# Optimization experiments

Hardware: AMD Instinct MI355X
Metric: run time of the kernel (lower is better)

The kernel has to match this reference:

```python
import jax, jax.numpy as jnp
import numpy as np

B, C, H, W = 2, 256, 64, 64
HEADS = 8
HEAD_DIM = C // HEADS  # 32
INNER = HEADS * HEAD_DIM  # 256
GROUPS = 32
EPS = 1e-5


def groupnorm(x, w, b):
    # x: [B, C, H, W]; normalize over (C//G, H, W) within each of G groups
    Bx, Cx, Hx, Wx = x.shape
    xg = x.reshape(Bx, GROUPS, -1)
    mu = xg.mean(axis=-1, keepdims=True)
    var = xg.var(axis=-1, keepdims=True)
    xn = ((xg - mu) * jax.lax.rsqrt(var + EPS)).reshape(Bx, Cx, Hx, Wx)
    return xn * w[:, None, None] + b[:, None, None]


def setup_inputs() -> dict:
    key = jax.random.key(0)
    k0, k1, k2 = jax.random.split(key, 3)
    x = jax.random.normal(k0, (B, C, H, W), dtype=jnp.float32)
    gn_weight = jnp.ones((C,), dtype=jnp.float32)
    gn_bias = jnp.zeros((C,), dtype=jnp.float32)
    # 1x1 conv weights (kernel dims squeezed): [out_ch, in_ch]
    w_qkv = jax.random.normal(k1, (3 * INNER, C), dtype=jnp.float32) * 0.02
    w_out = jax.random.normal(k2, (C, INNER), dtype=jnp.float32) * 0.02
    return {"x": x, "gn_weight": gn_weight, "gn_bias": gn_bias,
            "w_qkv": w_qkv, "w_out": w_out}


def reference(x, gn_weight, gn_bias, w_qkv, w_out):
    Bx, Cx, Hx, Wx = x.shape
    N = Hx * Wx
    scale = HEAD_DIM ** -0.5
    xn = groupnorm(x, gn_weight, gn_bias)
    # 1x1 conv == channel matmul
    qkv = jnp.einsum('oc,bchw->bohw', w_qkv, xn)  # [B, 3*INNER, H, W]
    q, k, v = jnp.split(qkv, 3, axis=1)
    # 'b (h d) x y -> b h (x y) d'
    def to_heads(t):
        return t.reshape(Bx, HEADS, HEAD_DIM, N).transpose(0, 1, 3, 2)  # bhnd
    q, k, v = to_heads(q), to_heads(k), to_heads(v)
    sim = jnp.einsum('bhid,bhjd->bhij', q, k) * scale  # [B, h, N, N]
    attn = jax.nn.softmax(sim, axis=-1)
    o = jnp.einsum('bhij,bhjd->bhid', attn, v)  # [B, h, N, d]
    # 'b h (x y) d -> b (h d) x y'
    o = o.transpose(0, 1, 3, 2).reshape(Bx, INNER, Hx, Wx)
    out = jnp.einsum('co,bohw->bchw', w_out, o)
    return x + out
```

## Files before the change

kernel.cpp:

```cpp
#include <hip/hip_runtime.h>
#include <hip/hip_bf16.h>

#define BATCH 2
#define CH 256
#define HW 4096
#define HEADS 8
#define HDIM 32
#define GROUPS 32
#define EPS 1e-5f
#define SCALE 0.17677669529663687f
#define QSCALE (0.17677669529663687f * 1.4426950408889634f)

typedef short s16x8 __attribute__((ext_vector_type(8)));
typedef float floatx4 __attribute__((ext_vector_type(4)));
typedef unsigned short ushort_t;
typedef unsigned int uint_t;

static __device__ __forceinline__ ushort_t f2bf(float f) {
    __hip_bfloat16 h = __float2bfloat16(f);
    return *reinterpret_cast<ushort_t*>(&h);
}

static __device__ __forceinline__ uint_t pk2(float lo, float hi) {
    return __builtin_amdgcn_perm(__float_as_uint(hi), __float_as_uint(lo), 0x07060302u);
}

static __device__ __forceinline__ void gload_lds16(const ushort_t* g, ushort_t* l) {
    __builtin_amdgcn_global_load_lds((const __attribute__((address_space(1))) void*)g,
                                     (__attribute__((address_space(3))) void*)l, 16, 0, 0);
}

__global__ void gn_stats(const float* __restrict__ x, float* __restrict__ stats) {
    int bg = blockIdx.x;
    const float4* xv = (const float4*)(x + (size_t)bg * 8 * HW);
    int t = threadIdx.x;
    float s = 0.f, ss = 0.f;
    for (int i = t; i < 8192; i += 256) {
        float4 v = xv[i];
        s  += v.x + v.y + v.z + v.w;
        ss += v.x*v.x + v.y*v.y + v.z*v.z + v.w*v.w;
    }
    #pragma unroll
    for (int off = 32; off; off >>= 1) {
        s  += __shfl_down(s, off);
        ss += __shfl_down(ss, off);
    }
    __shared__ float rs[4], rss[4];
    int wave = t >> 6;
    if ((t & 63) == 0) { rs[wave] = s; rss[wave] = ss; }
    __syncthreads();
    if (t == 0) {
        s  = rs[0] + rs[1] + rs[2] + rs[3];
        ss = rss[0] + rss[1] + rss[2] + rss[3];
        float mu  = s / 32768.f;
        float var = ss / 32768.f - mu * mu;
        stats[bg * 2]     = mu;
        stats[bg * 2 + 1] = rsqrtf(var + EPS);
    }
}

__global__ void norm_transpose(const float* __restrict__ x, const float* __restrict__ stats,
                               const float* __restrict__ gw, const float* __restrict__ gb,
                               ushort_t* __restrict__ xn) {
    __shared__ ushort_t tile[64][40];
    int b = blockIdx.z, c0 = blockIdx.y * 32, n0 = blockIdx.x * 64;
    int t = threadIdx.x;
    #pragma unroll
    for (int i = 0; i < 8; i++) {
        int idx = i * 256 + t;
        int c = idx >> 6, n = idx & 63;
        int cc = c0 + c;
        float mu   = stats[(b * GROUPS + (cc >> 3)) * 2];
        float rstd = stats[(b * GROUPS + (cc >> 3)) * 2 + 1];
        float v = x[((size_t)b * CH + cc) * HW + n0 + n];
        v = (v - mu) * rstd * gw[cc] + gb[cc];
        tile[n][c] = f2bf(v);
    }
    __syncthreads();
    int n = t >> 2, chk = t & 3;
    uint4 val = *(const uint4*)&tile[n][chk * 8];
    *(uint4*)(xn + ((size_t)(b * HW + n0 + n)) * CH + c0 + chk * 8) = val;
}

__global__ void qkv_gemm(const ushort_t* __restrict__ xn, const float* __restrict__ wqkv,
                         ushort_t* __restrict__ qo, ushort_t* __restrict__ ko,
                         ushort_t* __restrict__ vo) {
    __shared__ ushort_t Al[64][40];
    __shared__ ushort_t Bl[64][40];
    int b = blockIdx.z;
    int n0 = blockIdx.x * 64, o0 = blockIdx.y * 64;
    int t = threadIdx.x, lane = t & 63, wave = t >> 6;
    int lr = lane & 15, lk = lane >> 4;
    floatx4 acc[4] = {};
    for (int k0 = 0; k0 < 256; k0 += 32) {
        int row = t >> 2, chk = t & 3;
        *(uint4*)&Al[row][chk * 8] =
            *(const uint4*)(xn + ((size_t)(b * HW + n0 + row)) * CH + k0 + chk * 8);
        const float* wsrc = wqkv + (size_t)(o0 + row) * CH + k0 + chk * 8;
        ushort_t tmp[8];
        #pragma unroll
        for (int j = 0; j < 8; j++) tmp[j] = f2bf(wsrc[j]);
        *(uint4*)&Bl[row][chk * 8] = *(uint4*)tmp;
        __syncthreads();
        s16x8 af = *(const s16x8*)&Al[wave * 16 + lr][lk * 8];
        #pragma unroll
        for (int ct = 0; ct < 4; ct++) {
            s16x8 bf = *(const s16x8*)&Bl[ct * 16 + lr][lk * 8];
            acc[ct] = __builtin_amdgcn_mfma_f32_16x16x32_bf16(af, bf, acc[ct], 0, 0, 0);
        }
        __syncthreads();
    }
    #pragma unroll
    for (int ct = 0; ct < 4; ct++) {
        int o = o0 + ct * 16 + lr;
        int sel = o >> 8;
        int h = (o >> 5) & 7;
        int d = o & 31;
        int nrow0 = n0 + wave * 16 + (lk << 2);
        if (sel == 0) {
            #pragma unroll
            for (int r = 0; r < 4; r++)
                qo[(((size_t)(b * HEADS + h)) * HW + nrow0 + r) * HDIM + d] =
                    f2bf(acc[ct][r] * QSCALE);
        } else if (sel == 1) {
            #pragma unroll
            for (int r = 0; r < 4; r++) {
                int tt = (nrow0 + r) & 63;
                int sg = 4 * ((tt >> 3) & 3) + 16 * ((((tt >> 2) & 1) << 1) | ((tt >> 5) & 1)) + (tt & 3);
                ko[(((size_t)(b * HEADS + h)) * HW + n0 + sg) * HDIM + d] = f2bf(acc[ct][r]);
            }
        } else {
            ushort_t pk[4];
            #pragma unroll
            for (int r = 0; r < 4; r++) pk[r] = f2bf(acc[ct][r]);
            *(uint2*)&vo[(((size_t)(b * HEADS + h)) * HDIM + d) * HW + nrow0] = *(uint2*)pk;
        }
    }
}

__global__ void __launch_bounds__(256, 4)
attn4(const ushort_t* __restrict__ qg, const ushort_t* __restrict__ kg,
      const ushort_t* __restrict__ vg, ushort_t* __restrict__ og) {
    __shared__ ushort_t Kl[2][2048];
    __shared__ ushort_t Vl[2][2048];
    const int bh = blockIdx.y;
    const int n0 = blockIdx.x * 64;
    const int t = threadIdx.x;
    const int lane = t & 63, w = t >> 6;
    const int lr = lane & 15, lk = lane >> 4;

    const ushort_t* kb = kg + (size_t)bh * HW * HDIM;
    const ushort_t* vb = vg + (size_t)bh * HDIM * HW;

    const int lrr = t & 15, lkk = (t >> 4) & 3, wv = t >> 6;
    const ushort_t* gk = kb + ((wv << 4) + lrr) * HDIM + lkk * 8;
    const ushort_t* gv = vb + (size_t)(((t >> 7) << 4) + lrr) * HW + ((t >> 6) & 1) * 32 + lkk * 8;
    ushort_t* kd0 = &Kl[0][wv << 9]; ushort_t* kd1 = &Kl[1][wv << 9];
    ushort_t* vd0 = &Vl[0][wv << 9]; ushort_t* vd1 = &Vl[1][wv << 9];

    s16x8 qf = *(const s16x8*)(qg + ((size_t)bh * HW + n0 + w * 16 + lr) * HDIM + lk * 8);

    const s16x8 onesf = {0x3F80, 0x3F80, 0x3F80, 0x3F80, 0x3F80, 0x3F80, 0x3F80, 0x3F80};
    const floatx4 zf = {};
    floatx4 oacc[2] = {};
    floatx4 Lacc = {};

    gload_lds16(gk, kd0);
    gload_lds16(gv, vd0);
    gk += 64 * HDIM; gv += 64;
    asm volatile("s_waitcnt vmcnt(0)" ::: "memory");
    __syncthreads();

    for (int kt = 0; kt < 64; kt++) {
        const int cur = kt & 1;
        const ushort_t* Kb = cur ? Kl[1] : Kl[0];
        const ushort_t* Vb = cur ? Vl[1] : Vl[0];
        if (kt < 63) {
            gload_lds16(gk, cur ? kd0 : kd1);
            gload_lds16(gv, cur ? vd0 : vd1);
            gk += 64 * HDIM; gv += 64;
        }
        floatx4 sim[4];
        __builtin_amdgcn_s_setprio(1);
#pragma unroll
        for (int ct = 0; ct < 4; ct++) {
            s16x8 kf = *(const s16x8*)(Kb + ct * 512 + lane * 8);
            sim[ct] = __builtin_amdgcn_mfma_f32_16x16x32_bf16(kf, qf, zf, 0, 0, 0);
        }
        __builtin_amdgcn_s_setprio(0);
        s16x8 vf[4];
#pragma unroll
        for (int i = 0; i < 4; i++)
            vf[i] = *(const s16x8*)(Vb + i * 512 + lane * 8);

        float p[4][4];
#pragma unroll
        for (int ct = 0; ct < 4; ct++)
#pragma unroll
            for (int r = 0; r < 4; r++) p[ct][r] = __builtin_amdgcn_exp2f(sim[ct][r]);
        s16x8 pf[2];
#pragma unroll
        for (int s = 0; s < 2; s++) {
            union { uint_t u[4]; s16x8 v; } pu;
            pu.u[0] = pk2(p[s][0], p[s][1]);
            pu.u[1] = pk2(p[s][2], p[s][3]);
            pu.u[2] = pk2(p[s + 2][0], p[s + 2][1]);
            pu.u[3] = pk2(p[s + 2][2], p[s + 2][3]);
            pf[s] = pu.v;
        }
        __builtin_amdgcn_s_setprio(1);
#pragma unroll
        for (int s = 0; s < 2; s++) {
            oacc[0] = __builtin_amdgcn_mfma_f32_16x16x32_bf16(vf[s],     pf[s], oacc[0], 0, 0, 0);
            oacc[1] = __builtin_amdgcn_mfma_f32_16x16x32_bf16(vf[2 + s], pf[s], oacc[1], 0, 0, 0);
            Lacc    = __builtin_amdgcn_mfma_f32_16x16x32_bf16(onesf,     pf[s], Lacc,    0, 0, 0);
        }
        __builtin_amdgcn_s_setprio(0);
        asm volatile("s_waitcnt vmcnt(0)" ::: "memory");
        __syncthreads();
    }

    const int b = bh >> 3, h = bh & 7;
    float inv = 1.0f / Lacc[0];
    int n = n0 + w * 16 + lr;
#pragma unroll
    for (int ct2 = 0; ct2 < 2; ct2++) {
        uint_t lo = (uint_t)f2bf(oacc[ct2][0] * inv) | ((uint_t)f2bf(oacc[ct2][1] * inv) << 16);
        uint_t hi = (uint_t)f2bf(oacc[ct2][2] * inv) | ((uint_t)f2bf(oacc[ct2][3] * inv) << 16);
        uint2 val = {lo, hi};
        *(uint2*)(og + ((size_t)b * HW + n) * CH + h * 32 + ct2 * 16 + lk * 4) = val;
    }
}

__global__ void proj_res(const ushort_t* __restrict__ oa, const float* __restrict__ wout,
                         const float* __restrict__ x, float* __restrict__ out) {
    __shared__ ushort_t Al[64][40];
    __shared__ ushort_t Bl[64][40];
    int m0 = blockIdx.x * 64;
    int c0 = blockIdx.y * 64;
    int t = threadIdx.x, lane = t & 63, wave = t >> 6;
    int lr = lane & 15, lk = lane >> 4;
    floatx4 acc[4] = {};
    for (int k0 = 0; k0 < 256; k0 += 32) {
        int row = t >> 2, chk = t & 3;
        *(uint4*)&Al[row][chk * 8] =
            *(const uint4*)(oa + (size_t)(m0 + row) * CH + k0 + chk * 8);
        const float* wsrc = wout + (size_t)(c0 + row) * CH + k0 + chk * 8;
        ushort_t tmp[8];
        #pragma unroll
        for (int j = 0; j < 8; j++) tmp[j] = f2bf(wsrc[j]);
        *(uint4*)&Bl[row][chk * 8] = *(uint4*)tmp;
        __syncthreads();
        s16x8 af = *(const s16x8*)&Al[wave * 16 + lr][lk * 8];
        #pragma unroll
        for (int ct = 0; ct < 4; ct++) {
            s16x8 bf = *(const s16x8*)&Bl[ct * 16 + lr][lk * 8];
            acc[ct] = __builtin_amdgcn_mfma_f32_16x16x32_bf16(af, bf, acc[ct], 0, 0, 0);
        }
        __syncthreads();
    }
    int mrow0 = m0 + wave * 16 + (lk << 2);
    int b = mrow0 >> 12;
    int n = mrow0 & 4095;
    #pragma unroll
    for (int ct = 0; ct < 4; ct++) {
        int c = c0 + ct * 16 + lr;
        const float4 xv = *(const float4*)(x + ((size_t)(b * CH + c)) * HW + n);
        float4 ov;
        ov.x = acc[ct][0] + xv.x;
        ov.y = acc[ct][1] + xv.y;
        ov.z = acc[ct][2] + xv.z;
        ov.w = acc[ct][3] + xv.w;
        *(float4*)(out + ((size_t)(b * CH + c)) * HW + n) = ov;
    }
}

extern "C" void kernel_launch(void* const* d_in, const int* in_sizes, int n_in,
                              void* d_out, int out_size, void* d_ws, size_t ws_size,
                              hipStream_t stream) {
    const float* x    = (const float*)d_in[0];
    const float* gw   = (const float*)d_in[1];
    const float* gb   = (const float*)d_in[2];
    const float* wqkv = (const float*)d_in[3];
    const float* wout = (const float*)d_in[4];
    float* out = (float*)d_out;

    char* ws = (char*)d_ws;
    float* stats = (float*)ws;
    ushort_t* xn = (ushort_t*)(ws + 512);
    size_t per = (size_t)BATCH * HW * CH;
    ushort_t* q  = xn + per;
    ushort_t* k  = q + per;
    ushort_t* v  = k + per;
    ushort_t* oa = v + per;

    gn_stats<<<64, 256, 0, stream>>>(x, stats);
    norm_transpose<<<dim3(64, 8, 2), 256, 0, stream>>>(x, stats, gw, gb, xn);
    qkv_gemm<<<dim3(64, 12, 2), 256, 0, stream>>>(xn, wqkv, q, k, v);
    attn4<<<dim3(64, 16), 256, 0, stream>>>(q, k, v, oa);
    proj_res<<<dim3(128, 4), 256, 0, stream>>>(oa, wout, x, out);
}
```

Baseline: 88.27 us.

## Pre-convert weights to bf16 once and deepen attention K/V prefetch to four stages

Adds a small kernel that converts the QKV and output-projection weights to bf16 in workspace once per call, so the two GEMMs load bf16 directly instead of converting fp32 per tile. Replaces the attention kernel's double-buffered K/V staging with a 4-buffer ring that keeps two tiles in flight, waiting with vmcnt(2) instead of draining all loads each iteration. This adds one extra launch and doubles the attention kernel's LDS use, which could reduce occupancy at 4 blocks per CU.

```diff
diff --git a/kernel.cpp b/kernel.cpp
--- a/kernel.cpp
+++ b/kernel.cpp
@@ -28,6 +28,19 @@
 static __device__ __forceinline__ void gload_lds16(const ushort_t* g, ushort_t* l) {
     __builtin_amdgcn_global_load_lds((const __attribute__((address_space(1))) void*)g,
                                      (__attribute__((address_space(3))) void*)l, 16, 0, 0);
+}
+
+__global__ void wcvt(const float* __restrict__ wq, const float* __restrict__ wo,
+                     ushort_t* __restrict__ dst) {
+    int i = blockIdx.x * 256 + threadIdx.x;
+    float4 v = (i < 49152) ? ((const float4*)wq)[i] : ((const float4*)wo)[i - 49152];
+    uint2 o;
+    o.x = pk2(v.x, v.y);
+    o.y = pk2(v.z, v.w);
+    ushort_t p[4] = {f2bf(v.x), f2bf(v.y), f2bf(v.z), f2bf(v.w)};
+    o.x = (uint_t)p[0] | ((uint_t)p[1] << 16);
+    o.y = (uint_t)p[2] | ((uint_t)p[3] << 16);
+    *(uint2*)&dst[(size_t)i * 4] = o;
 }
 
 __global__ void gn_stats(const float* __restrict__ x, float* __restrict__ stats) {
@@ -82,7 +95,7 @@
     *(uint4*)(xn + ((size_t)(b * HW + n0 + n)) * CH + c0 + chk * 8) = val;
 }
 
-__global__ void qkv_gemm(const ushort_t* __restrict__ xn, const float* __restrict__ wqkv,
+__global__ void qkv_gemm(const ushort_t* __restrict__ xn, const ushort_t* __restrict__ wqb,
                          ushort_t* __restrict__ qo, ushort_t* __restrict__ ko,
                          ushort_t* __restrict__ vo) {
     __shared__ ushort_t Al[64][40];
@@ -96,11 +109,8 @@
         int row = t >> 2, chk = t & 3;
         *(uint4*)&Al[row][chk * 8] =
             *(const uint4*)(xn + ((size_t)(b * HW + n0 + row)) * CH + k0 + chk * 8);
-        const float* wsrc = wqkv + (size_t)(o0 + row) * CH + k0 + chk * 8;
-        ushort_t tmp[8];
-        #pragma unroll
-        for (int j = 0; j < 8; j++) tmp[j] = f2bf(wsrc[j]);
-        *(uint4*)&Bl[row][chk * 8] = *(uint4*)tmp;
+        *(uint4*)&Bl[row][chk * 8] =
+            *(const uint4*)(wqb + (size_t)(o0 + row) * CH + k0 + chk * 8);
         __syncthreads();
         s16x8 af = *(const s16x8*)&Al[wave * 16 + lr][lk * 8];
         #pragma unroll
@@ -139,10 +149,10 @@
 }
 
 __global__ void __launch_bounds__(256, 4)
-attn4(const ushort_t* __restrict__ qg, const ushort_t* __restrict__ kg,
+attn5(const ushort_t* __restrict__ qg, const ushort_t* __restrict__ kg,
       const ushort_t* __restrict__ vg, ushort_t* __restrict__ og) {
-    __shared__ ushort_t Kl[2][2048];
-    __shared__ ushort_t Vl[2][2048];
+    __shared__ ushort_t Kl[4][2048];
+    __shared__ ushort_t Vl[4][2048];
     const int bh = blockIdx.y;
     const int n0 = blockIdx.x * 64;
     const int t = threadIdx.x;
@@ -156,7 +166,9 @@
     const ushort_t* gk = kb + ((wv << 4) + lrr) * HDIM + lkk * 8;
     const ushort_t* gv = vb + (size_t)(((t >> 7) << 4) + lrr) * HW + ((t >> 6) & 1) * 32 + lkk * 8;
     ushort_t* kd0 = &Kl[0][wv << 9]; ushort_t* kd1 = &Kl[1][wv << 9];
+    ushort_t* kd2 = &Kl[2][wv << 9]; ushort_t* kd3 = &Kl[3][wv << 9];
     ushort_t* vd0 = &Vl[0][wv << 9]; ushort_t* vd1 = &Vl[1][wv << 9];
+    ushort_t* vd2 = &Vl[2][wv << 9]; ushort_t* vd3 = &Vl[3][wv << 9];
 
     s16x8 qf = *(const s16x8*)(qg + ((size_t)bh * HW + n0 + w * 16 + lr) * HDIM + lk * 8);
 
@@ -165,19 +177,11 @@
     floatx4 oacc[2] = {};
     floatx4 Lacc = {};
 
-    gload_lds16(gk, kd0);
-    gload_lds16(gv, vd0);
-    gk += 64 * HDIM; gv += 64;
-    asm volatile("s_waitcnt vmcnt(0)" ::: "memory");
-    __syncthreads();
-
-    for (int kt = 0; kt < 64; kt++) {
-        const int cur = kt & 1;
-        const ushort_t* Kb = cur ? Kl[1] : Kl[0];
-        const ushort_t* Vb = cur ? Vl[1] : Vl[0];
-        if (kt < 63) {
-            gload_lds16(gk, cur ? kd0 : kd1);
-            gload_lds16(gv, cur ? vd0 : vd1);
+    auto step = [&](const ushort_t* Kb, const ushort_t* Vb,
+                    ushort_t* kdn, ushort_t* vdn, bool dostage) {
+        if (dostage) {
+            gload_lds16(gk, kdn);
+            gload_lds16(gv, vdn);
             gk += 64 * HDIM; gv += 64;
         }
         floatx4 sim[4];
@@ -192,7 +196,6 @@
 #pragma unroll
         for (int i = 0; i < 4; i++)
             vf[i] = *(const s16x8*)(Vb + i * 512 + lane * 8);
-
         float p[4][4];
 #pragma unroll
         for (int ct = 0; ct < 4; ct++)
@@ -216,9 +219,27 @@
             Lacc    = __builtin_amdgcn_mfma_f32_16x16x32_bf16(onesf,     pf[s], Lacc,    0, 0, 0);
         }
         __builtin_amdgcn_s_setprio(0);
-        asm volatile("s_waitcnt vmcnt(0)" ::: "memory");
-        __syncthreads();
-    }
+    };
+
+#define W2 { asm volatile("s_waitcnt vmcnt(2)" ::: "memory"); __syncthreads(); }
+#define W0 { asm volatile("s_waitcnt vmcnt(0)" ::: "memory"); __syncthreads(); }
+
+    gload_lds16(gk, kd0); gload_lds16(gv, vd0); gk += 64 * HDIM; gv += 64;
+    gload_lds16(gk, kd1); gload_lds16(gv, vd1); gk += 64 * HDIM; gv += 64;
+    W2
+
+    for (int kt = 0; kt < 60; kt += 4) {
+        step(Kl[0], Vl[0], kd2, vd2, true); W2
+        step(Kl[1], Vl[1], kd3, vd3, true); W2
+        step(Kl[2], Vl[2], kd0, vd0, true); W2
+        step(Kl[3], Vl[3], kd1, vd1, true); W2
+    }
+    step(Kl[0], Vl[0], kd2, vd2, true); W2
+    step(Kl[1], Vl[1], kd3, vd3, true); W2
+    step(Kl[2], Vl[2], nullptr, nullptr, false); W0
+    step(Kl[3], Vl[3], nullptr, nullptr, false);
+#undef W2
+#undef W0
 
     const int b = bh >> 3, h = bh & 7;
     float inv = 1.0f / Lacc[0];
@@ -232,7 +253,7 @@
     }
 }
 
-__global__ void proj_res(const ushort_t* __restrict__ oa, const float* __restrict__ wout,
+__global__ void proj_res(const ushort_t* __restrict__ oa, const ushort_t* __restrict__ wob,
                          const float* __restrict__ x, float* __restrict__ out) {
     __shared__ ushort_t Al[64][40];
     __shared__ ushort_t Bl[64][40];
@@ -245,11 +266,8 @@
         int row = t >> 2, chk = t & 3;
         *(uint4*)&Al[row][chk * 8] =
             *(const uint4*)(oa + (size_t)(m0 + row) * CH + k0 + chk * 8);
-        const float* wsrc = wout + (size_t)(c0 + row) * CH + k0 + chk * 8;
-        ushort_t tmp[8];
-        #pragma unroll
-        for (int j = 0; j < 8; j++) tmp[j] = f2bf(wsrc[j]);
-        *(uint4*)&Bl[row][chk * 8] = *(uint4*)tmp;
+        *(uint4*)&Bl[row][chk * 8] =
+            *(const uint4*)(wob + (size_t)(c0 + row) * CH + k0 + chk * 8);
         __syncthreads();
         s16x8 af = *(const s16x8*)&Al[wave * 16 + lr][lk * 8];
         #pragma unroll
@@ -289,14 +307,17 @@
     float* stats = (float*)ws;
     ushort_t* xn = (ushort_t*)(ws + 512);
     size_t per = (size_t)BATCH * HW * CH;
-    ushort_t* q  = xn + per;
-    ushort_t* k  = q + per;
-    ushort_t* v  = k + per;
-    ushort_t* oa = v + per;
-
+    ushort_t* q   = xn + per;
+    ushort_t* k   = q + per;
+    ushort_t* v   = k + per;
+    ushort_t* oa  = v + per;
+    ushort_t* wqb = oa + per;
+    ushort_t* wob = wqb + 196608;
+
+    wcvt<<<256, 256, 0, stream>>>(wqkv, wout, wqb);
     gn_stats<<<64, 256, 0, stream>>>(x, stats);
     norm_transpose<<<dim3(64, 8, 2), 256, 0, stream>>>(x, stats, gw, gb, xn);
-    qkv_gemm<<<dim3(64, 12, 2), 256, 0, stream>>>(xn, wqkv, q, k, v);
-    attn4<<<dim3(64, 16), 256, 0, stream>>>(q, k, v, oa);
-    proj_res<<<dim3(128, 4), 256, 0, stream>>>(oa, wout, x, out);
-}
+    qkv_gemm<<<dim3(64, 12, 2), 256, 0, stream>>>(xn, wqb, q, k, v);
+    attn5<<<dim3(64, 16), 256, 0, stream>>>(q, k, v, oa);
+    proj_res<<<dim3(128, 4), 256, 0, stream>>>(oa, wob, x, out);
+}
```

Result: slower. 93.25 us (+5.6%).
